# Kernel tuning notes

Measured on AMD Instinct MI355X. Metric: run time of the kernel, lower is better.

## Reference

```python
import jax, jax.numpy as jnp
import numpy as np

B, FEAT_DIM, NUM_BANDS = 64, 512, 8
H_VAL, W_VAL = 1024, 1024


def setup_inputs() -> dict:
    key = jax.random.key(0)
    k1, k2, k3 = jax.random.split(key, 3)
    freq_feat = jax.random.normal(k1, (B, FEAT_DIM), dtype=jnp.float32)
    w = jax.random.normal(k2, (NUM_BANDS, FEAT_DIM), dtype=jnp.float32) * 0.05
    b = jax.random.normal(k3, (NUM_BANDS,), dtype=jnp.float32) * 0.05
    return {"freq_feat": freq_feat, "w": w, "b": b, "H": H_VAL, "W": W_VAL}


def reference(freq_feat, w, b, H, W):
    # MLP: Linear(feat_dim -> num_bands) + Softmax over bands
    logits = freq_feat @ w.T + b                      # [B, nb]
    band_weights = jax.nn.softmax(logits, axis=1)     # [B, nb]
    nb = band_weights.shape[1]

    # Radial frequency grid, shape [H, W//2+1]
    u = jnp.fft.rfftfreq(W).astype(freq_feat.dtype)
    v = jnp.fft.fftfreq(H).astype(freq_feat.dtype)
    v_grid, u_grid = jnp.meshgrid(v, u, indexing='ij')
    radius = jnp.sqrt(u_grid ** 2 + v_grid ** 2)
    max_r = radius.max()

    # Band membership masks for all bands at once: [nb, H, W//2+1]
    i = jnp.arange(nb, dtype=freq_feat.dtype)
    lower = max_r * (i / nb)
    upper = max_r * ((i + 1.0) / nb)
    masks = ((radius[None] >= lower[:, None, None]) &
             (radius[None] < upper[:, None, None])).astype(freq_feat.dtype)

    # Weighted sum over bands -> [B, 1, H, W//2+1]
    freq_mask = jnp.einsum('bn,nhw->bhw', band_weights, masks)
    return freq_mask[:, None, :, :]
```

## Files before the change

kernel.cpp:

```cpp
#include <hip/hip_runtime.h>
#include <math.h>

#define NB     8
#define BATCH  64
#define FEAT   512
#define HGT    1024
#define WHALF  513
#define PIX    (HGT * WHALF)
#define TOTAL  (BATCH * PIX)

#define MAX_R  0x1.6A09E6p-1f

__global__ void bw_kernel(const float* __restrict__ ff,
                          const float* __restrict__ w,
                          const float* __restrict__ bias,
                          float* __restrict__ bw) {
    const int b = blockIdx.x;
    const int t = threadIdx.x;

    float part[NB];
#pragma unroll
    for (int n = 0; n < NB; ++n) part[n] = 0.0f;

    for (int k = t; k < FEAT; k += 256) {
        float f = ff[b * FEAT + k];
#pragma unroll
        for (int n = 0; n < NB; ++n) part[n] += f * w[n * FEAT + k];
    }

#pragma unroll
    for (int n = 0; n < NB; ++n) {
#pragma unroll
        for (int off = 32; off > 0; off >>= 1)
            part[n] += __shfl_down(part[n], off);
    }

    __shared__ float red[4][NB];
    const int wave = t >> 6, lane = t & 63;
    if (lane == 0) {
#pragma unroll
        for (int n = 0; n < NB; ++n) red[wave][n] = part[n];
    }
    __syncthreads();

    if (t == 0) {
        float logit[NB], m = -1e30f;
#pragma unroll
        for (int n = 0; n < NB; ++n) {
            logit[n] = red[0][n] + red[1][n] + red[2][n] + red[3][n] + bias[n];
            m = fmaxf(m, logit[n]);
        }
        float s = 0.0f;
#pragma unroll
        for (int n = 0; n < NB; ++n) { logit[n] = expf(logit[n] - m); s += logit[n]; }
        const float inv = 1.0f / s;
#pragma unroll
        for (int n = 0; n < NB; ++n) bw[b * NB + n] = logit[n] * inv;
    }
}

__device__ __forceinline__ int band_of(int p) {
    const int h  = p / WHALF;
    const int wp = p - h * WHALF;
    const float u = (float)wp * 0.0009765625f;
    const int hv  = (h >= 512) ? (h - 1024) : h;
    const float v = (float)hv * 0.0009765625f;
    const float r = sqrtf(fmaf(u, u, v * v));

    int j = (int)(r * (8.0f / MAX_R));
    if (j > 8) j = 8;
    const float lo = MAX_R * ((float)j * 0.125f);
    if (r < lo) {
        --j;
    } else if (j < 8) {
        const float hi = MAX_R * ((float)(j + 1) * 0.125f);
        if (r >= hi) ++j;
    }
    return j;
}

__global__ void band_kernel(unsigned char* __restrict__ band) {
    const int p = blockIdx.x * blockDim.x + threadIdx.x;
    if (p >= PIX) return;
    band[p] = (unsigned char)band_of(p);
}

__global__ void __launch_bounds__(256)
out_kernel(const float* __restrict__ bw,
           const unsigned char* __restrict__ band,
           float* __restrict__ out) {
    __shared__ float sbw[BATCH * NB + NB];
    for (int i = threadIdx.x; i < BATCH * NB + NB; i += blockDim.x)
        sbw[i] = (i < BATCH * NB) ? bw[i] : 0.0f;
    __syncthreads();

    const int nq = TOTAL / 4;
    const int stride = gridDim.x * blockDim.x;
    for (int q = blockIdx.x * blockDim.x + threadIdx.x; q < nq; q += stride) {
        const int base = q * 4;
        const int b = base / PIX;
        const int p = base - b * PIX;
        const uchar4 j4 = *reinterpret_cast<const uchar4*>(band + p);
        const float* row = sbw + b * NB;
        float4 o;
        o.x = (j4.x < 8) ? row[j4.x] : 0.0f;
        o.y = (j4.y < 8) ? row[j4.y] : 0.0f;
        o.z = (j4.z < 8) ? row[j4.z] : 0.0f;
        o.w = (j4.w < 8) ? row[j4.w] : 0.0f;
        reinterpret_cast<float4*>(out)[q] = o;
    }
}

__global__ void __launch_bounds__(256)
out_fused_kernel(const float* __restrict__ bw, float* __restrict__ out) {
    __shared__ float sbw[BATCH * NB];
    for (int i = threadIdx.x; i < BATCH * NB; i += blockDim.x) sbw[i] = bw[i];
    __syncthreads();

    const int nq = TOTAL / 4;
    const int stride = gridDim.x * blockDim.x;
    for (int q = blockIdx.x * blockDim.x + threadIdx.x; q < nq; q += stride) {
        const int base = q * 4;
        const int b = base / PIX;
        const int p = base - b * PIX;
        const float* row = sbw + b * NB;
        float4 o;
        int j;
        j = band_of(p + 0); o.x = (j < 8) ? row[j] : 0.0f;
        j = band_of(p + 1); o.y = (j < 8) ? row[j] : 0.0f;
        j = band_of(p + 2); o.z = (j < 8) ? row[j] : 0.0f;
        j = band_of(p + 3); o.w = (j < 8) ? row[j] : 0.0f;
        reinterpret_cast<float4*>(out)[q] = o;
    }
}

extern "C" void kernel_launch(void* const* d_in, const int* in_sizes, int n_in,
                              void* d_out, int out_size, void* d_ws, size_t ws_size,
                              hipStream_t stream) {
    const float* ff   = (const float*)d_in[0];
    const float* w    = (const float*)d_in[1];
    const float* bias = (const float*)d_in[2];
    float* out = (float*)d_out;

    float* bw = (float*)d_ws;
    unsigned char* band = (unsigned char*)d_ws + 2048;

    bw_kernel<<<BATCH, 256, 0, stream>>>(ff, w, bias, bw);

    if (ws_size >= 2048 + (size_t)PIX) {
        band_kernel<<<(PIX + 255) / 256, 256, 0, stream>>>(band);
        out_kernel<<<2048, 256, 0, stream>>>(bw, band, out);
    } else {
        out_fused_kernel<<<2048, 256, 0, stream>>>(bw, out);
    }
}
```

Measured before the change: 147.4 us.

## Merge band and weight prep kernels; reuse band loads across batches with nontemporal stores

The softmax-weight kernel and the band-index kernel are merged into one prep launch, which removes one kernel launch. The output kernel now reads one uchar4 of band indices per thread and writes it to 8 batch images, so each index load is reused 8 times instead of once. Stores use nontemporal float4 writes. Each batch row is padded with a ninth zero entry so the branch on out-of-range bands goes away. The cost is more blocks, each doing a small fixed amount of work, and a shared-memory row stride of 9.

After: 150.1 us. No clear change (+1.8%).

```diff
diff --git a/kernel.cpp b/kernel.cpp
--- a/kernel.cpp
+++ b/kernel.cpp
@@ -11,19 +11,54 @@
 
 #define MAX_R  0x1.6A09E6p-1f
 
-__global__ void bw_kernel(const float* __restrict__ ff,
-                          const float* __restrict__ w,
-                          const float* __restrict__ bias,
-                          float* __restrict__ bw) {
-    const int b = blockIdx.x;
+typedef float vfloat4 __attribute__((ext_vector_type(4)));
+
+__device__ __forceinline__ int band_of(int p) {
+    const int h  = p / WHALF;
+    const int wp = p - h * WHALF;
+    const float u = (float)wp * 0.0009765625f;
+    const int hv  = (h >= 512) ? (h - 1024) : h;
+    const float v = (float)hv * 0.0009765625f;
+    const float r = sqrtf(fmaf(u, u, v * v));
+
+    int j = (int)(r * (8.0f / MAX_R));
+    if (j > 8) j = 8;
+    const float lo = MAX_R * ((float)j * 0.125f);
+    if (r < lo) {
+        --j;
+    } else if (j < 8) {
+        const float hi = MAX_R * ((float)(j + 1) * 0.125f);
+        if (r >= hi) ++j;
+    }
+    return j;
+}
+
+__global__ void __launch_bounds__(256)
+prep_kernel(const float* __restrict__ ff,
+            const float* __restrict__ w,
+            const float* __restrict__ bias,
+            float* __restrict__ bw,
+            unsigned char* __restrict__ band) {
     const int t = threadIdx.x;
 
+    if (blockIdx.x >= BATCH) {
+        const int p = (blockIdx.x - BATCH) * 1024 + t * 4;
+        uchar4 o;
+        o.x = (unsigned char)band_of(p + 0);
+        o.y = (unsigned char)band_of(p + 1);
+        o.z = (unsigned char)band_of(p + 2);
+        o.w = (unsigned char)band_of(p + 3);
+        *reinterpret_cast<uchar4*>(band + p) = o;
+        return;
+    }
+
+    const int b = blockIdx.x;
     float part[NB];
 #pragma unroll
     for (int n = 0; n < NB; ++n) part[n] = 0.0f;
 
     for (int k = t; k < FEAT; k += 256) {
-        float f = ff[b * FEAT + k];
+        const float f = ff[b * FEAT + k];
 #pragma unroll
         for (int n = 0; n < NB; ++n) part[n] += f * w[n * FEAT + k];
     }
@@ -59,39 +94,44 @@
     }
 }
 
-__device__ __forceinline__ int band_of(int p) {
-    const int h  = p / WHALF;
-    const int wp = p - h * WHALF;
-    const float u = (float)wp * 0.0009765625f;
-    const int hv  = (h >= 512) ? (h - 1024) : h;
-    const float v = (float)hv * 0.0009765625f;
-    const float r = sqrtf(fmaf(u, u, v * v));
-
-    int j = (int)(r * (8.0f / MAX_R));
-    if (j > 8) j = 8;
-    const float lo = MAX_R * ((float)j * 0.125f);
-    if (r < lo) {
-        --j;
-    } else if (j < 8) {
-        const float hi = MAX_R * ((float)(j + 1) * 0.125f);
-        if (r >= hi) ++j;
-    }
-    return j;
-}
-
-__global__ void band_kernel(unsigned char* __restrict__ band) {
-    const int p = blockIdx.x * blockDim.x + threadIdx.x;
-    if (p >= PIX) return;
-    band[p] = (unsigned char)band_of(p);
-}
-
 __global__ void __launch_bounds__(256)
 out_kernel(const float* __restrict__ bw,
            const unsigned char* __restrict__ band,
            float* __restrict__ out) {
-    __shared__ float sbw[BATCH * NB + NB];
-    for (int i = threadIdx.x; i < BATCH * NB + NB; i += blockDim.x)
-        sbw[i] = (i < BATCH * NB) ? bw[i] : 0.0f;
+    __shared__ float sbw[BATCH * 9];
+    for (int i = threadIdx.x; i < BATCH * 9; i += 256) {
+        const int b = i / 9, j = i - b * 9;
+        sbw[i] = (j < NB) ? bw[b * NB + j] : 0.0f;
+    }
+    __syncthreads();
+
+    const int chunk = blockIdx.x >> 3;
+    const int bg    = blockIdx.x & 7;
+    const int p     = chunk * 1024 + (int)threadIdx.x * 4;
+
+    const uchar4 j4 = *reinterpret_cast<const uchar4*>(band + p);
+
+    float* o = out + (size_t)(bg * 8) * PIX + p;
+#pragma unroll
+    for (int i = 0; i < 8; ++i) {
+        const float* row = sbw + (bg * 8 + i) * 9;
+        vfloat4 v;
+        v.x = row[j4.x];
+        v.y = row[j4.y];
+        v.z = row[j4.z];
+        v.w = row[j4.w];
+        __builtin_nontemporal_store(v, reinterpret_cast<vfloat4*>(o));
+        o += PIX;
+    }
+}
+
+__global__ void __launch_bounds__(256)
+out_fused_kernel(const float* __restrict__ bw, float* __restrict__ out) {
+    __shared__ float sbw[BATCH * 9];
+    for (int i = threadIdx.x; i < BATCH * 9; i += 256) {
+        const int b = i / 9, j = i - b * 9;
+        sbw[i] = (j < NB) ? bw[b * NB + j] : 0.0f;
+    }
     __syncthreads();
 
     const int nq = TOTAL / 4;
@@ -100,36 +140,12 @@
         const int base = q * 4;
         const int b = base / PIX;
         const int p = base - b * PIX;
-        const uchar4 j4 = *reinterpret_cast<const uchar4*>(band + p);
-        const float* row = sbw + b * NB;
+        const float* row = sbw + b * 9;
         float4 o;
-        o.x = (j4.x < 8) ? row[j4.x] : 0.0f;
-        o.y = (j4.y < 8) ? row[j4.y] : 0.0f;
-        o.z = (j4.z < 8) ? row[j4.z] : 0.0f;
-        o.w = (j4.w < 8) ? row[j4.w] : 0.0f;
-        reinterpret_cast<float4*>(out)[q] = o;
-    }
-}
-
-__global__ void __launch_bounds__(256)
-out_fused_kernel(const float* __restrict__ bw, float* __restrict__ out) {
-    __shared__ float sbw[BATCH * NB];
-    for (int i = threadIdx.x; i < BATCH * NB; i += blockDim.x) sbw[i] = bw[i];
-    __syncthreads();
-
-    const int nq = TOTAL / 4;
-    const int stride = gridDim.x * blockDim.x;
-    for (int q = blockIdx.x * blockDim.x + threadIdx.x; q < nq; q += stride) {
-        const int base = q * 4;
-        const int b = base / PIX;
-        const int p = base - b * PIX;
-        const float* row = sbw + b * NB;
-        float4 o;
-        int j;
-        j = band_of(p + 0); o.x = (j < 8) ? row[j] : 0.0f;
-        j = band_of(p + 1); o.y = (j < 8) ? row[j] : 0.0f;
-        j = band_of(p + 2); o.z = (j < 8) ? row[j] : 0.0f;
-        j = band_of(p + 3); o.w = (j < 8) ? row[j] : 0.0f;
+        o.x = row[band_of(p + 0)];
+        o.y = row[band_of(p + 1)];
+        o.z = row[band_of(p + 2)];
+        o.w = row[band_of(p + 3)];
         reinterpret_cast<float4*>(out)[q] = o;
     }
 }
@@ -145,12 +161,11 @@
     float* bw = (float*)d_ws;
     unsigned char* band = (unsigned char*)d_ws + 2048;
 
-    bw_kernel<<<BATCH, 256, 0, stream>>>(ff, w, bias, bw);
-
     if (ws_size >= 2048 + (size_t)PIX) {
-        band_kernel<<<(PIX + 255) / 256, 256, 0, stream>>>(band);
-        out_kernel<<<2048, 256, 0, stream>>>(bw, band, out);
+        prep_kernel<<<BATCH + PIX / 1024, 256, 0, stream>>>(ff, w, bias, bw, band);
+        out_kernel<<<(PIX / 1024) * 8, 256, 0, stream>>>(bw, band, out);
     } else {
+        prep_kernel<<<BATCH, 256, 0, stream>>>(ff, w, bias, bw, band);
         out_fused_kernel<<<2048, 256, 0, stream>>>(bw, out);
     }
 }
```
